# Kernel tuning notes

Hardware: AMD Instinct MI355X
Metric: run time of the kernel (lower is better)

## Reference

```python
import jax, jax.numpy as jnp
import numpy as np

B, S, C = 2, 4096, 640
HEADS = 10
DH = C // HEADS  # 64
SCALE = 1.0 / np.sqrt(DH).astype(np.float32)


def setup_inputs() -> dict:
    key = jax.random.key(0)
    ks = jax.random.split(key, 5)
    w_std = 0.02
    return {
        "hidden_states": jax.random.normal(ks[0], (B, S, C), dtype=jnp.float32),
        "Wq": jax.random.normal(ks[1], (C, C), dtype=jnp.float32) * w_std,
        "Wk": jax.random.normal(ks[2], (C, C), dtype=jnp.float32) * w_std,
        "Wv": jax.random.normal(ks[3], (C, C), dtype=jnp.float32) * w_std,
        "Wo": jax.random.normal(ks[4], (C, C), dtype=jnp.float32) * w_std,
        "b_out": jnp.zeros((C,), dtype=jnp.float32),
    }


def _split_heads(x):
    # [B, S, C] -> [B, H, S, Dh]
    b, s, c = x.shape
    return x.reshape(b, s, HEADS, DH).transpose(0, 2, 1, 3)


def reference(hidden_states, Wq, Wk, Wv, Wo, b_out):
    residual = hidden_states
    # Linear projections (torch nn.Linear: x @ W.T), to_q/k/v have no bias
    q = jnp.einsum("bsc,dc->bsd", hidden_states, Wq)
    k = jnp.einsum("bsc,dc->bsd", hidden_states, Wk)
    v = jnp.einsum("bsc,dc->bsd", hidden_states, Wv)
    q = _split_heads(q)  # [B, H, S, Dh]
    k = _split_heads(k)
    v = _split_heads(v)
    # get_attention_scores: scaled QK^T + softmax (full O(S^2) matrix)
    scores = jnp.einsum("bhqd,bhkd->bhqk", q, k) * SCALE
    probs = jax.nn.softmax(scores, axis=-1)
    out = jnp.einsum("bhqk,bhkd->bhqd", probs, v)  # [B, H, S, Dh]
    # batch_to_head_dim: [B, H, S, Dh] -> [B, S, C]
    out = out.transpose(0, 2, 1, 3).reshape(hidden_states.shape)
    # to_out[0] Linear (with bias), to_out[1] Dropout = identity at eval
    out = jnp.einsum("bsc,dc->bsd", out, Wo) + b_out
    # residual_connection=True, rescale_output_factor=1.0
    return out + residual
```

## Files before the change

kernel.cpp:

```cpp
#include <hip/hip_runtime.h>
#include <stdint.h>
#include <stddef.h>

#define Bsz 2
#define Ssz 4096
#define Csz 640
#define Hn 10
#define Dh 64
#define NSPLIT 4
#define QROWS 81920

typedef __attribute__((ext_vector_type(8))) short bf16x8;
typedef __attribute__((ext_vector_type(4))) float f32x4;
typedef __attribute__((ext_vector_type(16))) float f32x16;

typedef __attribute__((address_space(1))) void as1_void;
typedef __attribute__((address_space(3))) void as3_void;

__device__ __forceinline__ void async16(const void* g, void* l) {
  __builtin_amdgcn_global_load_lds((as1_void*)(g), (as3_void*)(l), 16, 0, 0);
}

__device__ __forceinline__ ushort f2bf(float f) {
  union { float f; uint32_t u; } v; v.f = f;
  return (ushort)((v.u + 0x7FFFu + ((v.u >> 16) & 1u)) >> 16);
}

__device__ __forceinline__ uint32_t pack_bf16(float lo, float hi) {
  return __builtin_amdgcn_perm(__float_as_uint(hi), __float_as_uint(lo), 0x07060302u);
}

__device__ __forceinline__ float bf_lo(uint32_t u) {
  return __uint_as_float(u << 16);
}
__device__ __forceinline__ float bf_hi(uint32_t u) {
  return __uint_as_float(u & 0xFFFF0000u);
}

__device__ __forceinline__ float fast_exp2(float x) {
#if __has_builtin(__builtin_amdgcn_exp2f)
  return __builtin_amdgcn_exp2f(x);
#else
  return __exp2f(x);
#endif
}

#define QSCALE 0.1803368801111204f

__global__ __launch_bounds__(256) void cvt_bf16(const float* __restrict__ in,
                                                ushort* __restrict__ out, int n4) {
  int i = blockIdx.x * 256 + threadIdx.x;
  if (i < n4) {
    const float4 v = ((const float4*)in)[i];
    ushort4 o;
    o.x = f2bf(v.x); o.y = f2bf(v.y); o.z = f2bf(v.z); o.w = f2bf(v.w);
    ((ushort4*)out)[i] = o;
  }
}

__global__ __launch_bounds__(256) void cvt4_bf16(
    const float* __restrict__ i0, const float* __restrict__ i1,
    const float* __restrict__ i2, const float* __restrict__ i3,
    ushort* __restrict__ o0, ushort* __restrict__ o1,
    ushort* __restrict__ o2, ushort* __restrict__ o3, int n4) {
  const float* in = (blockIdx.y == 0) ? i0 : (blockIdx.y == 1) ? i1
                    : (blockIdx.y == 2) ? i2 : i3;
  ushort* out = (blockIdx.y == 0) ? o0 : (blockIdx.y == 1) ? o1
                : (blockIdx.y == 2) ? o2 : o3;
  int i = blockIdx.x * 256 + threadIdx.x;
  if (i < n4) {
    const float4 v = ((const float4*)in)[i];
    ushort4 o;
    o.x = f2bf(v.x); o.y = f2bf(v.y); o.z = f2bf(v.z); o.w = f2bf(v.w);
    ((ushort4*)out)[i] = o;
  }
}

template<int MODE>
__global__ __launch_bounds__(256) void gemm_k(
    const ushort* __restrict__ A, const ushort* __restrict__ W0,
    const ushort* __restrict__ W1, const ushort* __restrict__ W2,
    ushort* __restrict__ Qh, ushort* __restrict__ Kh, ushort* __restrict__ Vt,
    const float* __restrict__ bias, const float* __restrict__ residual,
    float* __restrict__ outf)
{
  __shared__ ushort As[128 * 64];
  __shared__ ushort Bs[128 * 64];
  const int t = threadIdx.x;
  const int lane = t & 63;
  const int w = t >> 6;
  const int quad = lane >> 4;
  const int l15 = lane & 15;
  const int m0 = blockIdx.x * 128;
  const int wub = t & ~63;

  int n0, mat;
  const ushort* W;
  if (MODE == 0) {
    mat = blockIdx.y / 5;
    n0 = (blockIdx.y % 5) * 128;
    W = (mat == 0) ? W0 : ((mat == 1) ? W1 : W2);
  } else {
    mat = 0;
    n0 = blockIdx.y * 128;
    W = W0;
  }
  const int qm = (w >> 1) * 64;
  const int qn = (w & 1) * 64;

  f32x4 acc[4][4];
  const f32x4 zero4 = {0.f, 0.f, 0.f, 0.f};
#pragma unroll
  for (int i = 0; i < 4; ++i)
#pragma unroll
    for (int j = 0; j < 4; ++j) acc[i][j] = zero4;

  for (int k0 = 0; k0 < Csz; k0 += 64) {
    __syncthreads();
#pragma unroll
    for (int s = 0; s < 4; ++s) {
      int L = s * 256 + t;
      int row = L >> 3, pc = L & 7;
      int c = pc ^ (row & 7);
      async16(A + (size_t)(m0 + row) * Csz + k0 + c * 8,
              (char*)As + (s * 256 + wub) * 16);
    }
#pragma unroll
    for (int s = 0; s < 4; ++s) {
      int L = s * 256 + t;
      int row = L >> 3, pc = L & 7;
      int c = pc ^ (row & 7);
      async16(W + (size_t)(n0 + row) * Csz + k0 + c * 8,
              (char*)Bs + (s * 256 + wub) * 16);
    }
    __syncthreads();
#pragma unroll
    for (int ks = 0; ks < 2; ++ks) {
      bf16x8 af[4], bfr[4];
#pragma unroll
      for (int i = 0; i < 4; ++i) {
        int row = qm + i * 16 + l15;
        int pc = (ks * 4 + quad) ^ (row & 7);
        af[i] = *(const bf16x8*)(As + row * 64 + pc * 8);
      }
#pragma unroll
      for (int j = 0; j < 4; ++j) {
        int row = qn + j * 16 + l15;
        int pc = (ks * 4 + quad) ^ (row & 7);
        bfr[j] = *(const bf16x8*)(Bs + row * 64 + pc * 8);
      }
#pragma unroll
      for (int i = 0; i < 4; ++i)
#pragma unroll
        for (int j = 0; j < 4; ++j)
          acc[i][j] = __builtin_amdgcn_mfma_f32_16x16x32_bf16(af[i], bfr[j], acc[i][j], 0, 0, 0);
    }
  }

  if (MODE == 0) {
    if (mat < 2) {
      ushort* __restrict__ dst = (mat == 0) ? Qh : Kh;
      const float sc = (mat == 0) ? QSCALE : 1.0f;
#pragma unroll
      for (int j = 0; j < 4; ++j) {
        int n = n0 + qn + j * 16 + l15;
        int h = n >> 6, dh = n & 63;
#pragma unroll
        for (int i = 0; i < 4; ++i) {
#pragma unroll
          for (int r = 0; r < 4; ++r) {
            int m = m0 + qm + i * 16 + quad * 4 + r;
            int b = m >> 12, sidx = m & 4095;
            dst[(((size_t)b * Hn + h) * Ssz + sidx) * Dh + dh] = f2bf(acc[i][j][r] * sc);
          }
        }
      }
    } else {
#pragma unroll
      for (int j = 0; j < 4; ++j) {
        int n = n0 + qn + j * 16 + l15;
        int h = n >> 6, dh = n & 63;
#pragma unroll
        for (int i = 0; i < 4; ++i) {
          int mb = m0 + qm + i * 16 + quad * 4;
          int b = mb >> 12, sidx = mb & 4095;
          ushort4 pk;
          pk.x = f2bf(acc[i][j][0]); pk.y = f2bf(acc[i][j][1]);
          pk.z = f2bf(acc[i][j][2]); pk.w = f2bf(acc[i][j][3]);
          *(ushort4*)(Vt + (((size_t)b * Hn + h) * Dh + dh) * Ssz + sidx) = pk;
        }
      }
    }
  } else {
#pragma unroll
    for (int j = 0; j < 4; ++j) {
      int n = n0 + qn + j * 16 + l15;
      float bs = bias[n];
#pragma unroll
      for (int i = 0; i < 4; ++i) {
#pragma unroll
        for (int r = 0; r < 4; ++r) {
          int m = m0 + qm + i * 16 + quad * 4 + r;
          size_t idx = (size_t)m * Csz + n;
          outf[idx] = acc[i][j][r] + bs + residual[idx];
        }
      }
    }
  }
}

__global__ __launch_bounds__(256, 2) void attn_k(
    const ushort* __restrict__ Qh, const ushort* __restrict__ Kh,
    const ushort* __restrict__ Vt, ushort* __restrict__ Opart,
    float* __restrict__ lpart)
{
  __shared__ ushort Ks[2][64 * 64];
  __shared__ ushort Vs[2][64 * 64];

  const int t = threadIdx.x;
  const int lane = t & 63;
  const int w = t >> 6;
  const int l31 = lane & 31;
  const int hi = lane >> 5;
  const int bh = blockIdx.y;
  const size_t qk_off = (size_t)bh * Ssz * Dh;
  const size_t v_off = (size_t)bh * Dh * Ssz;
  const int qbase = blockIdx.x * 256 + w * 64;
  const int kvbase = blockIdx.z * (Ssz / NSPLIT);

  bf16x8 qf[2][4];
#pragma unroll
  for (int qh = 0; qh < 2; ++qh) {
    int q = qbase + qh * 32 + l31;
#pragma unroll
    for (int ks = 0; ks < 4; ++ks)
      qf[qh][ks] = *(const bf16x8*)(Qh + qk_off + (size_t)q * Dh + ks * 16 + hi * 8);
  }

  f32x16 z16;
#pragma unroll
  for (int i = 0; i < 16; ++i) z16[i] = 0.f;

  f32x16 Oa[2][2];
#pragma unroll
  for (int qh = 0; qh < 2; ++qh)
#pragma unroll
    for (int mt = 0; mt < 2; ++mt) Oa[qh][mt] = z16;
  float lp[2] = {0.f, 0.f};

  const int row8 = lane >> 3;
  const int pcs = lane & 7;
#define STAGE(bi, kv)                                                          \
  {                                                                            \
    _Pragma("unroll") for (int s = 0; s < 2; ++s) {                            \
      int i = w * 2 + s;                                                       \
      int row = i * 8 + row8;                                                  \
      int c = pcs ^ (row & 7);                                                 \
      async16(Kh + qk_off + (size_t)(kvbase + (kv) + row) * Dh + c * 8,        \
              (char*)&Ks[bi][0] + i * 1024);                                   \
    }                                                                          \
    _Pragma("unroll") for (int s = 0; s < 2; ++s) {                            \
      int i = w * 2 + s;                                                       \
      int row = i * 8 + row8;                                                  \
      int c = pcs ^ (row & 7);                                                 \
      async16(Vt + v_off + (size_t)row * Ssz + kvbase + (kv) + c * 8,          \
              (char*)&Vs[bi][0] + i * 1024);                                   \
    }                                                                          \
  }

  STAGE(0, 0);

  const int NIT = (Ssz / NSPLIT) / 64;
  for (int it = 0; it < NIT; ++it) {
    const int cb = it & 1;
    asm volatile("s_barrier" ::: "memory");
    if (it + 1 < NIT) {
      STAGE(cb ^ 1, (it + 1) * 64);
      asm volatile("s_waitcnt vmcnt(4)" ::: "memory");
    } else {
      asm volatile("s_waitcnt vmcnt(0)" ::: "memory");
    }
    asm volatile("s_barrier" ::: "memory");

    const ushort* __restrict__ Kc = &Ks[cb][0];
    const ushort* __restrict__ Vc = &Vs[cb][0];

    uint32_t pk[2][2][8];
#pragma unroll
    for (int tau = 0; tau < 2; ++tau) {
      f32x16 Sq[2];
      int row = tau * 32 + l31;
#pragma unroll
      for (int ks = 0; ks < 4; ++ks) {
        int pc = (ks * 2 + hi) ^ (row & 7);
        bf16x8 kf = *(const bf16x8*)(Kc + row * 64 + pc * 8);
        Sq[0] = __builtin_amdgcn_mfma_f32_32x32x16_bf16(kf, qf[0][ks],
                                                        ks == 0 ? z16 : Sq[0], 0, 0, 0);
        Sq[1] = __builtin_amdgcn_mfma_f32_32x32x16_bf16(kf, qf[1][ks],
                                                        ks == 0 ? z16 : Sq[1], 0, 0, 0);
      }
#pragma unroll
      for (int qh = 0; qh < 2; ++qh) {
#pragma unroll
        for (int a = 0; a < 8; ++a) {
          float p0 = fast_exp2(Sq[qh][2 * a]);
          float p1 = fast_exp2(Sq[qh][2 * a + 1]);
          lp[qh] += p0 + p1;
          pk[qh][tau][a] = pack_bf16(p0, p1);
        }
      }
    }

#pragma unroll
    for (int ks2 = 0; ks2 < 4; ++ks2) {
      const int ts = ks2 >> 1;
      const int bA = (2 * ks2) & 3;
      const int bB = (2 * ks2 + 1) & 3;
      bf16x8 pf[2];
#pragma unroll
      for (int qh = 0; qh < 2; ++qh) {
        uint32_t xA0 = pk[qh][ts][2 * bA], xA1 = pk[qh][ts][2 * bA + 1];
        uint32_t xB0 = pk[qh][ts][2 * bB], xB1 = pk[qh][ts][2 * bB + 1];
        uint32_t own0 = hi ? xB0 : xA0, own1 = hi ? xB1 : xA1;
        uint32_t snd0 = hi ? xA0 : xB0, snd1 = hi ? xA1 : xB1;
        uint32_t rcv0 = (uint32_t)__shfl_xor((int)snd0, 32, 64);
        uint32_t rcv1 = (uint32_t)__shfl_xor((int)snd1, 32, 64);
        union { uint32_t u[4]; bf16x8 v; } pu;
        pu.u[0] = hi ? rcv0 : own0;
        pu.u[1] = hi ? rcv1 : own1;
        pu.u[2] = hi ? own0 : rcv0;
        pu.u[3] = hi ? own1 : rcv1;
        pf[qh] = pu.v;
      }
#pragma unroll
      for (int mt = 0; mt < 2; ++mt) {
        int row = mt * 32 + l31;
        int pc = (ks2 * 2 + hi) ^ (row & 7);
        bf16x8 vf = *(const bf16x8*)(Vc + row * 64 + pc * 8);
        Oa[0][mt] = __builtin_amdgcn_mfma_f32_32x32x16_bf16(vf, pf[0], Oa[0][mt], 0, 0, 0);
        Oa[1][mt] = __builtin_amdgcn_mfma_f32_32x32x16_bf16(vf, pf[1], Oa[1][mt], 0, 0, 0);
      }
    }
  }
#undef STAGE

  const size_t prow_base = (size_t)blockIdx.z * QROWS + (size_t)bh * Ssz;
#pragma unroll
  for (int qh = 0; qh < 2; ++qh) {
    float l_part = lp[qh];
    float l_tot = l_part + __shfl_xor(l_part, 32, 64);
    int q = qbase + qh * 32 + l31;
    if (hi == 0) lpart[prow_base + q] = l_tot;
    ushort* dst = Opart + (prow_base + q) * 64;
#pragma unroll
    for (int mt = 0; mt < 2; ++mt) {
#pragma unroll
      for (int g = 0; g < 4; ++g) {
        int dh0 = mt * 32 + 8 * g + 4 * hi;
        uint2 val;
        val.x = pack_bf16(Oa[qh][mt][4 * g + 0], Oa[qh][mt][4 * g + 1]);
        val.y = pack_bf16(Oa[qh][mt][4 * g + 2], Oa[qh][mt][4 * g + 3]);
        *(uint2*)(dst + dh0) = val;
      }
    }
  }
}

__global__ __launch_bounds__(256) void combine_k(
    const ushort* __restrict__ Opart, const float* __restrict__ lpart,
    ushort* __restrict__ attnb)
{
  int gid = blockIdx.x * 256 + threadIdx.x;
  int row = gid >> 4;
  int dh0 = (gid & 15) * 4;
  int bh = row >> 12, q = row & 4095;
  int b = bh / Hn, h = bh % Hn;
  float a0 = 0.f, a1 = 0.f, a2 = 0.f, a3 = 0.f, lsum = 0.f;
#pragma unroll
  for (int sp = 0; sp < NSPLIT; ++sp) {
    uint2 v = *(const uint2*)(Opart + ((size_t)sp * QROWS + row) * 64 + dh0);
    a0 += bf_lo(v.x); a1 += bf_hi(v.x);
    a2 += bf_lo(v.y); a3 += bf_hi(v.y);
    lsum += lpart[(size_t)sp * QROWS + row];
  }
  float inv = 1.0f / lsum;
  uint2 o;
  o.x = pack_bf16(a0 * inv, a1 * inv);
  o.y = pack_bf16(a2 * inv, a3 * inv);
  *(uint2*)(attnb + ((size_t)b * Ssz + q) * Csz + h * Dh + dh0) = o;
}

extern "C" void kernel_launch(void* const* d_in, const int* in_sizes, int n_in,
                              void* d_out, int out_size, void* d_ws, size_t ws_size,
                              hipStream_t stream) {
  (void)in_sizes; (void)n_in; (void)out_size; (void)ws_size;
  const float* hs = (const float*)d_in[0];
  const float* Wq = (const float*)d_in[1];
  const float* Wk = (const float*)d_in[2];
  const float* Wv = (const float*)d_in[3];
  const float* Wo = (const float*)d_in[4];
  const float* bo = (const float*)d_in[5];
  float* out = (float*)d_out;

  char* ws = (char*)d_ws;
  ushort* Xbf = (ushort*)(ws);
  ushort* Wqb = (ushort*)(ws + 10485760);
  ushort* Wkb = (ushort*)(ws + 10485760 + 819200);
  ushort* Wvb = (ushort*)(ws + 10485760 + 2 * 819200);
  ushort* Wob = (ushort*)(ws + 10485760 + 3 * 819200);
  ushort* Qh  = (ushort*)(ws + 13762560);
  ushort* Kh  = (ushort*)(ws + 13762560 + 10485760);
  ushort* Vt  = (ushort*)(ws + 13762560 + 2 * 10485760);
  ushort* attnb = (ushort*)(ws + 13762560 + 3 * 10485760);
  ushort* Opart = (ushort*)(ws + 55705600);
  float*  lpart = (float*)(ws + 55705600 + 41943040);

  hipLaunchKernelGGL(cvt_bf16, dim3(5120), dim3(256), 0, stream, hs, Xbf, 1310720);
  hipLaunchKernelGGL(cvt4_bf16, dim3(400, 4), dim3(256), 0, stream,
                     Wq, Wk, Wv, Wo, Wqb, Wkb, Wvb, Wob, 102400);

  hipLaunchKernelGGL((gemm_k<0>), dim3(64, 15), dim3(256), 0, stream,
                     Xbf, Wqb, Wkb, Wvb, Qh, Kh, Vt, (const float*)nullptr,
                     (const float*)nullptr, (float*)nullptr);
  hipLaunchKernelGGL(attn_k, dim3(16, 20, NSPLIT), dim3(256), 0, stream,
                     Qh, Kh, Vt, Opart, lpart);
  hipLaunchKernelGGL(combine_k, dim3(QROWS / 16), dim3(256), 0, stream,
                     Opart, lpart, attnb);
  hipLaunchKernelGGL((gemm_k<1>), dim3(64, 5), dim3(256), 0, stream,
                     attnb, Wob, (const ushort*)nullptr, (const ushort*)nullptr,
                     (ushort*)nullptr, (ushort*)nullptr, (ushort*)nullptr,
                     bo, hs, out);
}
```

Before: 253.2 us.

## Load K/V tiles directly from global into registers, dropping LDS staging

```diff
diff --git a/kernel.cpp b/kernel.cpp
--- a/kernel.cpp
+++ b/kernel.cpp
@@ -209,23 +209,18 @@
   }
 }
 
-__global__ __launch_bounds__(256, 2) void attn_k(
+__global__ __launch_bounds__(64, 3) void attn_k(
     const ushort* __restrict__ Qh, const ushort* __restrict__ Kh,
     const ushort* __restrict__ Vt, ushort* __restrict__ Opart,
     float* __restrict__ lpart)
 {
-  __shared__ ushort Ks[2][64 * 64];
-  __shared__ ushort Vs[2][64 * 64];
-
-  const int t = threadIdx.x;
-  const int lane = t & 63;
-  const int w = t >> 6;
+  const int lane = threadIdx.x;
   const int l31 = lane & 31;
   const int hi = lane >> 5;
   const int bh = blockIdx.y;
-  const size_t qk_off = (size_t)bh * Ssz * Dh;
-  const size_t v_off = (size_t)bh * Dh * Ssz;
-  const int qbase = blockIdx.x * 256 + w * 64;
+  const ushort* __restrict__ Kb = Kh + (size_t)bh * Ssz * Dh;
+  const ushort* __restrict__ Vb = Vt + (size_t)bh * Dh * Ssz;
+  const int qbase = blockIdx.x * 64;
   const int kvbase = blockIdx.z * (Ssz / NSPLIT);
 
   bf16x8 qf[2][4];
@@ -234,7 +229,8 @@
     int q = qbase + qh * 32 + l31;
 #pragma unroll
     for (int ks = 0; ks < 4; ++ks)
-      qf[qh][ks] = *(const bf16x8*)(Qh + qk_off + (size_t)q * Dh + ks * 16 + hi * 8);
+      qf[qh][ks] = *(const bf16x8*)(Qh + (size_t)bh * Ssz * Dh +
+                                    (size_t)q * Dh + ks * 16 + hi * 8);
   }
 
   f32x16 z16;
@@ -248,101 +244,71 @@
     for (int mt = 0; mt < 2; ++mt) Oa[qh][mt] = z16;
   float lp[2] = {0.f, 0.f};
 
-  const int row8 = lane >> 3;
-  const int pcs = lane & 7;
-#define STAGE(bi, kv)                                                          \
-  {                                                                            \
-    _Pragma("unroll") for (int s = 0; s < 2; ++s) {                            \
-      int i = w * 2 + s;                                                       \
-      int row = i * 8 + row8;                                                  \
-      int c = pcs ^ (row & 7);                                                 \
-      async16(Kh + qk_off + (size_t)(kvbase + (kv) + row) * Dh + c * 8,        \
-              (char*)&Ks[bi][0] + i * 1024);                                   \
-    }                                                                          \
-    _Pragma("unroll") for (int s = 0; s < 2; ++s) {                            \
-      int i = w * 2 + s;                                                       \
-      int row = i * 8 + row8;                                                  \
-      int c = pcs ^ (row & 7);                                                 \
-      async16(Vt + v_off + (size_t)row * Ssz + kvbase + (kv) + c * 8,          \
-              (char*)&Vs[bi][0] + i * 1024);                                   \
-    }                                                                          \
-  }
-
-  STAGE(0, 0);
-
   const int NIT = (Ssz / NSPLIT) / 64;
   for (int it = 0; it < NIT; ++it) {
-    const int cb = it & 1;
-    asm volatile("s_barrier" ::: "memory");
-    if (it + 1 < NIT) {
-      STAGE(cb ^ 1, (it + 1) * 64);
-      asm volatile("s_waitcnt vmcnt(4)" ::: "memory");
-    } else {
-      asm volatile("s_waitcnt vmcnt(0)" ::: "memory");
-    }
-    asm volatile("s_barrier" ::: "memory");
-
-    const ushort* __restrict__ Kc = &Ks[cb][0];
-    const ushort* __restrict__ Vc = &Vs[cb][0];
-
-    uint32_t pk[2][2][8];
+    const int kvoff = kvbase + it * 64;
 #pragma unroll
     for (int tau = 0; tau < 2; ++tau) {
-      f32x16 Sq[2];
-      int row = tau * 32 + l31;
-#pragma unroll
-      for (int ks = 0; ks < 4; ++ks) {
-        int pc = (ks * 2 + hi) ^ (row & 7);
-        bf16x8 kf = *(const bf16x8*)(Kc + row * 64 + pc * 8);
-        Sq[0] = __builtin_amdgcn_mfma_f32_32x32x16_bf16(kf, qf[0][ks],
-                                                        ks == 0 ? z16 : Sq[0], 0, 0, 0);
-        Sq[1] = __builtin_amdgcn_mfma_f32_32x32x16_bf16(kf, qf[1][ks],
-                                                        ks == 0 ? z16 : Sq[1], 0, 0, 0);
-      }
+      bf16x8 kf[4];
+#pragma unroll
+      for (int ks = 0; ks < 4; ++ks)
+        kf[ks] = *(const bf16x8*)(Kb + (size_t)(kvoff + tau * 32 + l31) * Dh +
+                                  ks * 16 + hi * 8);
+      bf16x8 vf[2][2];
+#pragma unroll
+      for (int ks2l = 0; ks2l < 2; ++ks2l)
+#pragma unroll
+        for (int mt = 0; mt < 2; ++mt)
+          vf[ks2l][mt] = *(const bf16x8*)(Vb + (size_t)(mt * 32 + l31) * Ssz +
+                                          kvoff + tau * 32 + ks2l * 16 + hi * 8);
+
+      uint32_t pk[2][8];
 #pragma unroll
       for (int qh = 0; qh < 2; ++qh) {
+        f32x16 Sq;
+#pragma unroll
+        for (int ks = 0; ks < 4; ++ks)
+          Sq = __builtin_amdgcn_mfma_f32_32x32x16_bf16(kf[ks], qf[qh][ks],
+                                                       ks == 0 ? z16 : Sq, 0, 0, 0);
 #pragma unroll
         for (int a = 0; a < 8; ++a) {
-          float p0 = fast_exp2(Sq[qh][2 * a]);
-          float p1 = fast_exp2(Sq[qh][2 * a + 1]);
+          float p0 = fast_exp2(Sq[2 * a]);
+          float p1 = fast_exp2(Sq[2 * a + 1]);
           lp[qh] += p0 + p1;
-          pk[qh][tau][a] = pack_bf16(p0, p1);
-        }
-      }
-    }
-
-#pragma unroll
-    for (int ks2 = 0; ks2 < 4; ++ks2) {
-      const int ts = ks2 >> 1;
-      const int bA = (2 * ks2) & 3;
-      const int bB = (2 * ks2 + 1) & 3;
-      bf16x8 pf[2];
-#pragma unroll
-      for (int qh = 0; qh < 2; ++qh) {
-        uint32_t xA0 = pk[qh][ts][2 * bA], xA1 = pk[qh][ts][2 * bA + 1];
-        uint32_t xB0 = pk[qh][ts][2 * bB], xB1 = pk[qh][ts][2 * bB + 1];
-        uint32_t own0 = hi ? xB0 : xA0, own1 = hi ? xB1 : xA1;
-        uint32_t snd0 = hi ? xA0 : xB0, snd1 = hi ? xA1 : xB1;
-        uint32_t rcv0 = (uint32_t)__shfl_xor((int)snd0, 32, 64);
-        uint32_t rcv1 = (uint32_t)__shfl_xor((int)snd1, 32, 64);
-        union { uint32_t u[4]; bf16x8 v; } pu;
-        pu.u[0] = hi ? rcv0 : own0;
-        pu.u[1] = hi ? rcv1 : own1;
-        pu.u[2] = hi ? own0 : rcv0;
-        pu.u[3] = hi ? own1 : rcv1;
-        pf[qh] = pu.v;
-      }
-#pragma unroll
-      for (int mt = 0; mt < 2; ++mt) {
-        int row = mt * 32 + l31;
-        int pc = (ks2 * 2 + hi) ^ (row & 7);
-        bf16x8 vf = *(const bf16x8*)(Vc + row * 64 + pc * 8);
-        Oa[0][mt] = __builtin_amdgcn_mfma_f32_32x32x16_bf16(vf, pf[0], Oa[0][mt], 0, 0, 0);
-        Oa[1][mt] = __builtin_amdgcn_mfma_f32_32x32x16_bf16(vf, pf[1], Oa[1][mt], 0, 0, 0);
-      }
-    }
-  }
-#undef STAGE
+          pk[qh][a] = pack_bf16(p0, p1);
+        }
+      }
+
+#pragma unroll
+      for (int ks2l = 0; ks2l < 2; ++ks2l) {
+        const int bA = (2 * ks2l) & 3;
+        const int bB = (2 * ks2l + 1) & 3;
+        bf16x8 pf[2];
+#pragma unroll
+        for (int qh = 0; qh < 2; ++qh) {
+          uint32_t xA0 = pk[qh][2 * bA], xA1 = pk[qh][2 * bA + 1];
+          uint32_t xB0 = pk[qh][2 * bB], xB1 = pk[qh][2 * bB + 1];
+          uint32_t own0 = hi ? xB0 : xA0, own1 = hi ? xB1 : xA1;
+          uint32_t snd0 = hi ? xA0 : xB0, snd1 = hi ? xA1 : xB1;
+          uint32_t rcv0 = (uint32_t)__shfl_xor((int)snd0, 32, 64);
+          uint32_t rcv1 = (uint32_t)__shfl_xor((int)snd1, 32, 64);
+          union { uint32_t u[4]; bf16x8 v; } pu;
+          pu.u[0] = hi ? rcv0 : own0;
+          pu.u[1] = hi ? rcv1 : own1;
+          pu.u[2] = hi ? own0 : rcv0;
+          pu.u[3] = hi ? own1 : rcv1;
+          pf[qh] = pu.v;
+        }
+#pragma unroll
+        for (int mt = 0; mt < 2; ++mt) {
+          Oa[0][mt] = __builtin_amdgcn_mfma_f32_32x32x16_bf16(vf[ks2l][mt], pf[0],
+                                                              Oa[0][mt], 0, 0, 0);
+          Oa[1][mt] = __builtin_amdgcn_mfma_f32_32x32x16_bf16(vf[ks2l][mt], pf[1],
+                                                              Oa[1][mt], 0, 0, 0);
+        }
+      }
+    }
+  }
 
   const size_t prow_base = (size_t)blockIdx.z * QROWS + (size_t)bh * Ssz;
 #pragma unroll
@@ -422,7 +388,7 @@
   hipLaunchKernelGGL((gemm_k<0>), dim3(64, 15), dim3(256), 0, stream,
                      Xbf, Wqb, Wkb, Wvb, Qh, Kh, Vt, (const float*)nullptr,
                      (const float*)nullptr, (float*)nullptr);
-  hipLaunchKernelGGL(attn_k, dim3(16, 20, NSPLIT), dim3(256), 0, stream,
+  hipLaunchKernelGGL(attn_k, dim3(64, 20, NSPLIT), dim3(64), 0, stream,
                      Qh, Kh, Vt, Opart, lpart);
   hipLaunchKernelGGL(combine_k, dim3(QROWS / 16), dim3(256), 0, stream,
                      Opart, lpart, attnb);
```

Result: slower. 507.2 us (+100.4%).

## Fuse Q/K/V projections per tile to share A loads; use permlane32 swap

Applied to the files above, without the earlier changes.

```diff
diff --git a/kernel.cpp b/kernel.cpp
--- a/kernel.cpp
+++ b/kernel.cpp
@@ -16,6 +16,10 @@
 
 typedef __attribute__((address_space(1))) void as1_void;
 typedef __attribute__((address_space(3))) void as3_void;
+
+#if __has_builtin(__builtin_amdgcn_permlane32_swap)
+#define HAVE_PLSWAP 1
+#endif
 
 __device__ __forceinline__ void async16(const void* g, void* l) {
   __builtin_amdgcn_global_load_lds((as1_void*)(g), (as3_void*)(l), 16, 0, 0);
@@ -76,11 +80,126 @@
   }
 }
 
-template<int MODE>
-__global__ __launch_bounds__(256) void gemm_k(
+__global__ __launch_bounds__(256) void gemm_qkv(
     const ushort* __restrict__ A, const ushort* __restrict__ W0,
     const ushort* __restrict__ W1, const ushort* __restrict__ W2,
-    ushort* __restrict__ Qh, ushort* __restrict__ Kh, ushort* __restrict__ Vt,
+    ushort* __restrict__ Qh, ushort* __restrict__ Kh, ushort* __restrict__ Vt)
+{
+  __shared__ ushort As[128 * 64];
+  __shared__ ushort Bs[3][64 * 64];
+  const int t = threadIdx.x;
+  const int lane = t & 63;
+  const int w = t >> 6;
+  const int quad = lane >> 4;
+  const int l15 = lane & 15;
+  const int m0 = blockIdx.x * 128;
+  const int n0 = blockIdx.y * 64;
+  const int wub = t & ~63;
+  const int qm = (w >> 1) * 64;
+  const int qn = (w & 1) * 32;
+
+  const ushort* const Ws[3] = {W0, W1, W2};
+
+  f32x4 acc[3][4][2];
+  const f32x4 zero4 = {0.f, 0.f, 0.f, 0.f};
+#pragma unroll
+  for (int mat = 0; mat < 3; ++mat)
+#pragma unroll
+    for (int i = 0; i < 4; ++i)
+#pragma unroll
+      for (int j = 0; j < 2; ++j) acc[mat][i][j] = zero4;
+
+  for (int k0 = 0; k0 < Csz; k0 += 64) {
+    __syncthreads();
+#pragma unroll
+    for (int s = 0; s < 4; ++s) {
+      int L = s * 256 + t;
+      int row = L >> 3, pc = L & 7;
+      int c = pc ^ (row & 7);
+      async16(A + (size_t)(m0 + row) * Csz + k0 + c * 8,
+              (char*)As + (s * 256 + wub) * 16);
+    }
+#pragma unroll
+    for (int mat = 0; mat < 3; ++mat) {
+#pragma unroll
+      for (int s = 0; s < 2; ++s) {
+        int L = s * 256 + t;
+        int row = L >> 3, pc = L & 7;
+        int c = pc ^ (row & 7);
+        async16(Ws[mat] + (size_t)(n0 + row) * Csz + k0 + c * 8,
+                (char*)&Bs[mat][0] + (s * 256 + wub) * 16);
+      }
+    }
+    __syncthreads();
+#pragma unroll
+    for (int ks = 0; ks < 2; ++ks) {
+      bf16x8 af[4];
+#pragma unroll
+      for (int i = 0; i < 4; ++i) {
+        int row = qm + i * 16 + l15;
+        int pc = (ks * 4 + quad) ^ (row & 7);
+        af[i] = *(const bf16x8*)(As + row * 64 + pc * 8);
+      }
+#pragma unroll
+      for (int mat = 0; mat < 3; ++mat) {
+        bf16x8 bf2[2];
+#pragma unroll
+        for (int j = 0; j < 2; ++j) {
+          int row = qn + j * 16 + l15;
+          int pc = (ks * 4 + quad) ^ (row & 7);
+          bf2[j] = *(const bf16x8*)(&Bs[mat][row * 64 + pc * 8]);
+        }
+#pragma unroll
+        for (int i = 0; i < 4; ++i)
+#pragma unroll
+          for (int j = 0; j < 2; ++j)
+            acc[mat][i][j] = __builtin_amdgcn_mfma_f32_16x16x32_bf16(
+                af[i], bf2[j], acc[mat][i][j], 0, 0, 0);
+      }
+    }
+  }
+
+#pragma unroll
+  for (int mat = 0; mat < 3; ++mat) {
+    if (mat < 2) {
+      ushort* __restrict__ dst = (mat == 0) ? Qh : Kh;
+      const float sc = (mat == 0) ? QSCALE : 1.0f;
+#pragma unroll
+      for (int j = 0; j < 2; ++j) {
+        int n = n0 + qn + j * 16 + l15;
+        int h = n >> 6, dh = n & 63;
+#pragma unroll
+        for (int i = 0; i < 4; ++i) {
+#pragma unroll
+          for (int r = 0; r < 4; ++r) {
+            int m = m0 + qm + i * 16 + quad * 4 + r;
+            int b = m >> 12, sidx = m & 4095;
+            dst[(((size_t)b * Hn + h) * Ssz + sidx) * Dh + dh] =
+                f2bf(acc[mat][i][j][r] * sc);
+          }
+        }
+      }
+    } else {
+#pragma unroll
+      for (int j = 0; j < 2; ++j) {
+        int n = n0 + qn + j * 16 + l15;
+        int h = n >> 6, dh = n & 63;
+#pragma unroll
+        for (int i = 0; i < 4; ++i) {
+          int mb = m0 + qm + i * 16 + quad * 4;
+          int b = mb >> 12, sidx = mb & 4095;
+          ushort4 pk4;
+          pk4.x = f2bf(acc[2][i][j][0]); pk4.y = f2bf(acc[2][i][j][1]);
+          pk4.z = f2bf(acc[2][i][j][2]); pk4.w = f2bf(acc[2][i][j][3]);
+          *(ushort4*)(Vt + (((size_t)b * Hn + h) * Dh + dh) * Ssz + sidx) = pk4;
+        }
+      }
+    }
+  }
+}
+
+__global__ __launch_bounds__(256) void gemm_out(
+    const ushort* __restrict__ A, const ushort* __restrict__ W0,
     const float* __restrict__ bias, const float* __restrict__ residual,
     float* __restrict__ outf)
 {
@@ -92,19 +211,8 @@
   const int quad = lane >> 4;
   const int l15 = lane & 15;
   const int m0 = blockIdx.x * 128;
+  const int n0 = blockIdx.y * 128;
   const int wub = t & ~63;
-
-  int n0, mat;
-  const ushort* W;
-  if (MODE == 0) {
-    mat = blockIdx.y / 5;
-    n0 = (blockIdx.y % 5) * 128;
-    W = (mat == 0) ? W0 : ((mat == 1) ? W1 : W2);
-  } else {
-    mat = 0;
-    n0 = blockIdx.y * 128;
-    W = W0;
-  }
   const int qm = (w >> 1) * 64;
   const int qn = (w & 1) * 64;
 
@@ -130,7 +238,7 @@
       int L = s * 256 + t;
       int row = L >> 3, pc = L & 7;
       int c = pc ^ (row & 7);
-      async16(W + (size_t)(n0 + row) * Csz + k0 + c * 8,
+      async16(W0 + (size_t)(n0 + row) * Csz + k0 + c * 8,
               (char*)Bs + (s * 256 + wub) * 16);
     }
     __syncthreads();
@@ -157,53 +265,17 @@
     }
   }
 
-  if (MODE == 0) {
-    if (mat < 2) {
-      ushort* __restrict__ dst = (mat == 0) ? Qh : Kh;
-      const float sc = (mat == 0) ? QSCALE : 1.0f;
-#pragma unroll
-      for (int j = 0; j < 4; ++j) {
-        int n = n0 + qn + j * 16 + l15;
-        int h = n >> 6, dh = n & 63;
-#pragma unroll
-        for (int i = 0; i < 4; ++i) {
-#pragma unroll
-          for (int r = 0; r < 4; ++r) {
-            int m = m0 + qm + i * 16 + quad * 4 + r;
-            int b = m >> 12, sidx = m & 4095;
-            dst[(((size_t)b * Hn + h) * Ssz + sidx) * Dh + dh] = f2bf(acc[i][j][r] * sc);
-          }
-        }
-      }
-    } else {
-#pragma unroll
-      for (int j = 0; j < 4; ++j) {
-        int n = n0 + qn + j * 16 + l15;
-        int h = n >> 6, dh = n & 63;
-#pragma unroll
-        for (int i = 0; i < 4; ++i) {
-          int mb = m0 + qm + i * 16 + quad * 4;
-          int b = mb >> 12, sidx = mb & 4095;
-          ushort4 pk;
-          pk.x = f2bf(acc[i][j][0]); pk.y = f2bf(acc[i][j][1]);
-          pk.z = f2bf(acc[i][j][2]); pk.w = f2bf(acc[i][j][3]);
-          *(ushort4*)(Vt + (((size_t)b * Hn + h) * Dh + dh) * Ssz + sidx) = pk;
-        }
-      }
-    }
-  } else {
-#pragma unroll
-    for (int j = 0; j < 4; ++j) {
-      int n = n0 + qn + j * 16 + l15;
-      float bs = bias[n];
-#pragma unroll
-      for (int i = 0; i < 4; ++i) {
-#pragma unroll
-        for (int r = 0; r < 4; ++r) {
-          int m = m0 + qm + i * 16 + quad * 4 + r;
-          size_t idx = (size_t)m * Csz + n;
-          outf[idx] = acc[i][j][r] + bs + residual[idx];
-        }
+#pragma unroll
+  for (int j = 0; j < 4; ++j) {
+    int n = n0 + qn + j * 16 + l15;
+    float bs = bias[n];
+#pragma unroll
+    for (int i = 0; i < 4; ++i) {
+#pragma unroll
+      for (int r = 0; r < 4; ++r) {
+        int m = m0 + qm + i * 16 + quad * 4 + r;
+        size_t idx = (size_t)m * Csz + n;
+        outf[idx] = acc[i][j][r] + bs + residual[idx];
       }
     }
   }
@@ -321,15 +393,22 @@
       for (int qh = 0; qh < 2; ++qh) {
         uint32_t xA0 = pk[qh][ts][2 * bA], xA1 = pk[qh][ts][2 * bA + 1];
         uint32_t xB0 = pk[qh][ts][2 * bB], xB1 = pk[qh][ts][2 * bB + 1];
+        union { uint32_t u[4]; bf16x8 v; } pu;
+#if defined(HAVE_PLSWAP)
+        pu.u[0] = __builtin_amdgcn_permlane32_swap(xA0, xA0, false, false)[0];
+        pu.u[1] = __builtin_amdgcn_permlane32_swap(xA1, xA1, false, false)[0];
+        pu.u[2] = __builtin_amdgcn_permlane32_swap(xB0, xB0, false, false)[1];
+        pu.u[3] = __builtin_amdgcn_permlane32_swap(xB1, xB1, false, false)[1];
+#else
         uint32_t own0 = hi ? xB0 : xA0, own1 = hi ? xB1 : xA1;
         uint32_t snd0 = hi ? xA0 : xB0, snd1 = hi ? xA1 : xB1;
         uint32_t rcv0 = (uint32_t)__shfl_xor((int)snd0, 32, 64);
         uint32_t rcv1 = (uint32_t)__shfl_xor((int)snd1, 32, 64);
-        union { uint32_t u[4]; bf16x8 v; } pu;
         pu.u[0] = hi ? rcv0 : own0;
         pu.u[1] = hi ? rcv1 : own1;
         pu.u[2] = hi ? own0 : rcv0;
         pu.u[3] = hi ? own1 : rcv1;
+#endif
         pf[qh] = pu.v;
       }
 #pragma unroll
@@ -419,15 +498,12 @@
   hipLaunchKernelGGL(cvt4_bf16, dim3(400, 4), dim3(256), 0, stream,
                      Wq, Wk, Wv, Wo, Wqb, Wkb, Wvb, Wob, 102400);
 
-  hipLaunchKernelGGL((gemm_k<0>), dim3(64, 15), dim3(256), 0, stream,
-                     Xbf, Wqb, Wkb, Wvb, Qh, Kh, Vt, (const float*)nullptr,
-                     (const float*)nullptr, (float*)nullptr);
+  hipLaunchKernelGGL(gemm_qkv, dim3(64, 10), dim3(256), 0, stream,
+                     Xbf, Wqb, Wkb, Wvb, Qh, Kh, Vt);
   hipLaunchKernelGGL(attn_k, dim3(16, 20, NSPLIT), dim3(256), 0, stream,
                      Qh, Kh, Vt, Opart, lpart);
   hipLaunchKernelGGL(combine_k, dim3(QROWS / 16), dim3(256), 0, stream,
                      Opart, lpart, attnb);
-  hipLaunchKernelGGL((gemm_k<1>), dim3(64, 5), dim3(256), 0, stream,
-                     attnb, Wob, (const ushort*)nullptr, (const ushort*)nullptr,
-                     (ushort*)nullptr, (ushort*)nullptr, (ushort*)nullptr,
-                     bo, hs, out);
-}
+  hipLaunchKernelGGL(gemm_out, dim3(64, 5), dim3(256), 0, stream,
+                     attnb, Wob, bo, hs, out);
+}
```

After: 267.1 us. 5.5% more time.
